# Kernel tuning notes

Measured on AMD Instinct MI355X. Metric: run time of the kernel, lower is better.

The kernel has to match this reference:

```python
import jax, jax.numpy as jnp
import numpy as np

B, T_TEXT, T_MEL = 8, 256, 1024
VOCAB, MEL, H = 256, 80, 512
NH, HD = 8, 64  # MultiheadAttention: 8 heads, head_dim 64


def _linear(x, w, b):
    return x @ w.T + b


def _lstm(x, w_ih, w_hh, b_ih, b_hh, reverse=False):
    # torch LSTM, gate order i,f,g,o; x: [B,T,Din] -> [B,T,H]
    xg = jnp.einsum('bti,gi->btg', x, w_ih) + b_ih  # precompute input contributions
    h0 = jnp.zeros((x.shape[0], w_hh.shape[1]), x.dtype)

    def step(carry, xt):
        h, c = carry
        g = xt + h @ w_hh.T + b_hh
        i, f, gg, o = jnp.split(g, 4, axis=-1)
        c = jax.nn.sigmoid(f) * c + jax.nn.sigmoid(i) * jnp.tanh(gg)
        h = jax.nn.sigmoid(o) * jnp.tanh(c)
        return (h, c), h

    _, hs = jax.lax.scan(step, (h0, h0), jnp.swapaxes(xg, 0, 1), reverse=reverse)
    return jnp.swapaxes(hs, 0, 1)


def _length_regulate(enc, durations, max_len):
    # Vectorized equivalent of the nested python loop: token j owns output
    # positions [cum[j-1], cum[j]); padded positions are zero, mask True=pad.
    dur = jnp.round(durations).astype(jnp.int32)
    cum = jnp.cumsum(dur, axis=1)                              # [B,T_text]
    pos = jnp.arange(max_len)                                  # [max_len]
    idx = jax.vmap(lambda c: jnp.searchsorted(c, pos, side='right'))(cum)
    pad_mask = pos[None, :] >= cum[:, -1:]                     # True = padded
    idx = jnp.minimum(idx, enc.shape[1] - 1)
    exp = jnp.take_along_axis(enc, idx[..., None], axis=1)     # [B,max_len,H]
    exp = exp * (~pad_mask)[..., None].astype(enc.dtype)
    return exp, pad_mask


def setup_inputs() -> dict:
    key = jax.random.key(0)
    ks = jax.random.split(key, 40)

    def rn(k, shape, scale=0.02):
        return jax.random.normal(k, shape, jnp.float32) * scale

    inp = {}
    inp['phoneme_indices'] = jax.random.randint(ks[0], (B, T_TEXT), 0, VOCAB)
    inp['mel_specs'] = jax.random.normal(ks[1], (B, T_MEL, MEL), jnp.float32)
    inp['phoneme_durations'] = jax.random.randint(ks[2], (B, T_TEXT), 0, 8).astype(jnp.float32)
    # parameters
    inp['emb'] = rn(ks[3], (VOCAB, H), 1.0)
    inp['enc_w_ih_f'] = rn(ks[4], (4 * H, H))
    inp['enc_w_hh_f'] = rn(ks[5], (4 * H, H))
    inp['enc_b_ih_f'] = rn(ks[6], (4 * H,))
    inp['enc_b_hh_f'] = rn(ks[7], (4 * H,))
    inp['enc_w_ih_b'] = rn(ks[8], (4 * H, H))
    inp['enc_w_hh_b'] = rn(ks[9], (4 * H, H))
    inp['enc_b_ih_b'] = rn(ks[10], (4 * H,))
    inp['enc_b_hh_b'] = rn(ks[11], (4 * H,))
    inp['proj_w'] = rn(ks[12], (H, 2 * H))
    inp['proj_b'] = rn(ks[13], (H,))
    inp['dur_w1'] = rn(ks[14], (H, H))
    inp['dur_b1'] = rn(ks[15], (H,))
    inp['dur_w2'] = rn(ks[16], (H // 2, H))
    inp['dur_b2'] = rn(ks[17], (H // 2,))
    inp['dur_w3'] = rn(ks[18], (1, H // 2))
    inp['dur_b3'] = rn(ks[19], (1,))
    inp['mel_in_w'] = rn(ks[20], (H, MEL))
    inp['mel_in_b'] = rn(ks[21], (H,))
    inp['attn_in_w'] = rn(ks[22], (3 * H, H))
    inp['attn_in_b'] = rn(ks[23], (3 * H,))
    inp['attn_out_w'] = rn(ks[24], (H, H))
    inp['attn_out_b'] = rn(ks[25], (H,))
    inp['dec_w_ih'] = rn(ks[26], (4 * H, 2 * H))
    inp['dec_w_hh'] = rn(ks[27], (4 * H, H))
    inp['dec_b_ih'] = rn(ks[28], (4 * H,))
    inp['dec_b_hh'] = rn(ks[29], (4 * H,))
    inp['mel_out_w'] = rn(ks[30], (MEL, H))
    inp['mel_out_b'] = rn(ks[31], (MEL,))
    return inp


def reference(phoneme_indices, mel_specs, phoneme_durations, emb,
              enc_w_ih_f, enc_w_hh_f, enc_b_ih_f, enc_b_hh_f,
              enc_w_ih_b, enc_w_hh_b, enc_b_ih_b, enc_b_hh_b,
              proj_w, proj_b, dur_w1, dur_b1, dur_w2, dur_b2, dur_w3, dur_b3,
              mel_in_w, mel_in_b, attn_in_w, attn_in_b, attn_out_w, attn_out_b,
              dec_w_ih, dec_w_hh, dec_b_ih, dec_b_hh, mel_out_w, mel_out_b):
    b = phoneme_indices.shape[0]
    # encode_text (dropout = identity in eval)
    x = emb[phoneme_indices]                                   # [B,T_text,H]
    hf = _lstm(x, enc_w_ih_f, enc_w_hh_f, enc_b_ih_f, enc_b_hh_f)
    hb = _lstm(x, enc_w_ih_b, enc_w_hh_b, enc_b_ih_b, enc_b_hh_b, reverse=True)
    enc = _linear(jnp.concatenate([hf, hb], axis=-1), proj_w, proj_b)
    # duration predictor
    h1 = jax.nn.relu(_linear(enc, dur_w1, dur_b1))
    h2 = jax.nn.relu(_linear(h1, dur_w2, dur_b2))
    log_dur = _linear(h2, dur_w3, dur_b3)[..., 0]              # [B,T_text]
    # length regulation to mel length
    exp, pad_mask = _length_regulate(enc, phoneme_durations, mel_specs.shape[1])
    # teacher-forced decoder: queries depend only on shifted mel targets,
    # so the per-timestep attention loop == one batched MHA over all steps.
    mel_in = jnp.concatenate([jnp.zeros_like(mel_specs[:, :1]), mel_specs[:, :-1]], axis=1)
    q_in = _linear(mel_in, mel_in_w, mel_in_b)                 # [B,T_mel,H]
    wq, wk, wv = jnp.split(attn_in_w, 3, axis=0)
    bq, bk, bv = jnp.split(attn_in_b, 3, axis=0)
    q = _linear(q_in, wq, bq).reshape(b, -1, NH, HD)
    k = _linear(exp, wk, bk).reshape(b, -1, NH, HD)
    v = _linear(exp, wv, bv).reshape(b, -1, NH, HD)
    scores = jnp.einsum('bqhd,bkhd->bhqk', q, k) / np.sqrt(HD).astype(np.float32)
    scores = jnp.where(pad_mask[:, None, None, :], jnp.asarray(-1e9, scores.dtype), scores)
    attn = jax.nn.softmax(scores, axis=-1)
    ctx = jnp.einsum('bhqk,bkhd->bqhd', attn, v).reshape(b, -1, H)
    attended = _linear(ctx, attn_out_w, attn_out_b)
    # decoder LSTM over full sequence (the only true recurrence)
    dec_in = jnp.concatenate([q_in, attended], axis=-1)        # [B,T_mel,2H]
    dec_out = _lstm(dec_in, dec_w_ih, dec_w_hh, dec_b_ih, dec_b_hh)
    mel_pred = _linear(dec_out, mel_out_w, mel_out_b)          # [B,T_mel,MEL]
    return mel_pred, log_dur
```

## Files before the change

### kernel.cpp

```cpp
#include <hip/hip_runtime.h>
#include <hip/hip_bf16.h>


typedef unsigned short u16;
typedef unsigned int u32;
typedef unsigned long long u64;
typedef short short8 __attribute__((ext_vector_type(8)));
typedef float float4_ __attribute__((ext_vector_type(4)));

__device__ __forceinline__ u16 f2b16(float f) {
  u32 u = __float_as_uint(f);
  u = (u + 0x7FFF + ((u >> 16) & 1)) >> 16;
  return (u16)u;
}
__device__ __forceinline__ float b2f(u16 h) { return __uint_as_float((u32)h << 16); }
__device__ __forceinline__ float sigm(float x) { return 1.f / (1.f + __expf(-x)); }
__device__ __forceinline__ float tanh_(float x) { return 2.f / (1.f + __expf(-2.f * x)) - 1.f; }

__global__ void f2b_k(const float* __restrict__ s, u16* __restrict__ d, int n) {
  for (int i = blockIdx.x * 256 + threadIdx.x; i < n; i += gridDim.x * 256) d[i] = f2b16(s[i]);
}
__global__ void permconv_k(const float* __restrict__ s, u16* __restrict__ d, int K) {
  int row = blockIdx.x; int u = row >> 2, G = row & 3;
  const float* sr = s + (long)(G * 512 + u) * K;
  u16* dr = d + (long)row * K;
  for (int c = threadIdx.x; c < K; c += 256) dr[c] = f2b16(sr[c]);
}
__global__ void biascomb_k(const float* __restrict__ bih, const float* __restrict__ bhh,
                           float* __restrict__ out) {
  int r = blockIdx.x * 256 + threadIdx.x;
  int u = r >> 2, G = r & 3;
  out[r] = bih[G * 512 + u] + bhh[G * 512 + u];
}
__global__ void melinw_k(const float* __restrict__ s, u16* __restrict__ d) {
  int row = blockIdx.x, c = threadIdx.x;
  d[row * 128 + c] = (c < 80) ? f2b16(s[row * 80 + c]) : (u16)0;
}
__global__ void meloutw_k(const float* __restrict__ s, u16* __restrict__ d) {
  int row = blockIdx.x;
  for (int c = threadIdx.x; c < 512; c += 256)
    d[row * 512 + c] = (row < 80) ? f2b16(s[row * 512 + c]) : (u16)0;
}
__global__ void biaspad_k(const float* __restrict__ s, float* __restrict__ d) {
  int t = threadIdx.x;
  d[t] = (t < 80) ? s[t] : 0.f;
}
__global__ void embed_k(const int* __restrict__ pid, const float* __restrict__ emb,
                        u16* __restrict__ x) {
  int t = blockIdx.x, b = blockIdx.y;
  int row = pid[b * 256 + t];
  const float* e = emb + (long)row * 512;
  u16* xr = x + ((long)b * 256 + t) * 512;
  xr[threadIdx.x] = f2b16(e[threadIdx.x]);
  xr[threadIdx.x + 256] = f2b16(e[threadIdx.x + 256]);
}
__global__ void melin_k(const float* __restrict__ mel, u16* __restrict__ out) {
  int t = blockIdx.x, b = blockIdx.y, c = threadIdx.x;
  float v = (c < 80 && t > 0) ? mel[((long)b * 1024 + (t - 1)) * 80 + c] : 0.f;
  out[((long)b * 1024 + t) * 128 + c] = f2b16(v);
}
__global__ void cumsum_k(const float* __restrict__ dur, int* __restrict__ cum,
                         int* __restrict__ Lb) {
  int b = blockIdx.x, t = threadIdx.x;
  __shared__ int sd[256];
  sd[t] = __float2int_rn(dur[b * 256 + t]);
  __syncthreads();
  for (int o = 1; o < 256; o <<= 1) {
    int v = (t >= o) ? sd[t - o] : 0;
    __syncthreads();
    sd[t] += v;
    __syncthreads();
  }
  cum[b * 256 + t] = sd[t];
  if (t == 255) Lb[b] = min(sd[255], 1024);
}
__global__ void gather_k(const int* __restrict__ cum, const u16* __restrict__ enc,
                         u16* __restrict__ exp_) {
  int pos = blockIdx.x, b = blockIdx.y;
  const int* cb = cum + b * 256;
  int last = cb[255];
  u32 val = 0;
  if (pos < last) {
    int lo = 0, hi = 255;
    while (lo < hi) { int mid = (lo + hi) >> 1; if (cb[mid] > pos) hi = mid; else lo = mid + 1; }
    val = ((const u32*)(enc + ((long)b * 256 + lo) * 512))[threadIdx.x];
  }
  ((u32*)(exp_ + ((long)b * 1024 + pos) * 512))[threadIdx.x] = val;
}
__global__ void softmax_k(const float* __restrict__ sbuf, u16* __restrict__ P,
                          const int* __restrict__ Lb) {
  int qp = blockIdx.x, b = blockIdx.y;
  const float* s = sbuf + ((long)b * 1024 + qp) * 1024;
  u16* p = P + ((long)b * 1024 + qp) * 1024;
  int L = Lb[b];
  __shared__ float red[256];
  int tid = threadIdx.x;
  float m = -1e30f;
  for (int i = tid; i < L; i += 256) m = fmaxf(m, s[i]);
  red[tid] = m; __syncthreads();
  for (int o = 128; o > 0; o >>= 1) { if (tid < o) red[tid] = fmaxf(red[tid], red[tid + o]); __syncthreads(); }
  float mx = red[0];
  __syncthreads();
  float sm = 0.f;
  for (int i = tid; i < L; i += 256) sm += __expf(s[i] - mx);
  red[tid] = sm; __syncthreads();
  for (int o = 128; o > 0; o >>= 1) { if (tid < o) red[tid] += red[tid + o]; __syncthreads(); }
  float inv = 1.f / red[0];
  for (int i = tid; i < 1024; i += 256) {
    float v = (i < L) ? __expf(s[i] - mx) * inv : 0.f;
    p[i] = f2b16(v);
  }
}
__global__ void dur3_k(const u16* __restrict__ h2, const float* __restrict__ w3,
                       const float* __restrict__ b3, float* __restrict__ out) {
  int row = blockIdx.x * 4 + (threadIdx.x >> 6);
  int l = threadIdx.x & 63;
  const u16* hr = h2 + (long)row * 256;
  float s = 0.f;
  for (int i = 0; i < 4; i++) { int c = l * 4 + i; s += b2f(hr[c]) * w3[c]; }
  for (int o = 32; o > 0; o >>= 1) s += __shfl_down(s, o);
  if (l == 0) out[row] = s + b3[0];
}

__global__ __launch_bounds__(256) void gemm_bt(
    const u16* __restrict__ A, const u16* __restrict__ A2, int ksplit, int lda, int lda2, long sA,
    const u16* __restrict__ B, int ldb, long sB, void* __restrict__ Cv, int ldc, long sC,
    const float* __restrict__ bias, float alpha, int N, int K, int flags) {
  __shared__ u16 As[128 * 72];
  __shared__ u16 Bs[128 * 72];
  int z = blockIdx.z;
  const u16* Ab = A + (long)z * sA;
  const u16* A2b = A2 ? (A2 + (long)z * sA) : (const u16*)0;
  const u16* Bb = B + (long)z * sB;
  int m0 = blockIdx.x * 128, n0 = blockIdx.y * 128;
  int tid = threadIdx.x, wave = tid >> 6, lane = tid & 63;
  int wm = wave & 1, wn = wave >> 1;
  int nl = lane & 15, kb = (lane >> 4) * 8, ml = (lane >> 4) * 4;
  float4_ acc[4][4];
  for (int i = 0; i < 4; i++)
    for (int j = 0; j < 4; j++) { acc[i][j][0] = 0; acc[i][j][1] = 0; acc[i][j][2] = 0; acc[i][j][3] = 0; }
  int rr = tid >> 3, cc = (tid & 7) * 8;
  for (int k0 = 0; k0 < K; k0 += 64) {
    int gk = k0 + cc;
#pragma unroll
    for (int i = 0; i < 4; i++) {
      int row = rr + i * 32;
      const u16* sa = (gk < ksplit) ? (Ab + (long)(m0 + row) * lda + gk)
                                    : (A2b + (long)(m0 + row) * lda2 + (gk - ksplit));
      *(short8*)&As[row * 72 + cc] = *(const short8*)sa;
      *(short8*)&Bs[row * 72 + cc] = *(const short8*)(Bb + (long)(n0 + row) * ldb + gk);
    }
    __syncthreads();
#pragma unroll
    for (int kk = 0; kk < 64; kk += 32) {
      short8 af[4], bfr[4];
#pragma unroll
      for (int i = 0; i < 4; i++) af[i] = *(const short8*)&As[(wm * 64 + i * 16 + nl) * 72 + kk + kb];
#pragma unroll
      for (int i = 0; i < 4; i++) bfr[i] = *(const short8*)&Bs[(wn * 64 + i * 16 + nl) * 72 + kk + kb];
#pragma unroll
      for (int mi = 0; mi < 4; mi++)
#pragma unroll
        for (int ni = 0; ni < 4; ni++)
          acc[mi][ni] = __builtin_amdgcn_mfma_f32_16x16x32_bf16(af[mi], bfr[ni], acc[mi][ni], 0, 0, 0);
    }
    __syncthreads();
  }
  for (int ni = 0; ni < 4; ni++) {
    int n = n0 + wn * 64 + ni * 16 + nl;
    if (n >= N) continue;
    float bv = bias ? bias[n] : 0.f;
    for (int mi = 0; mi < 4; mi++) {
#pragma unroll
      for (int r = 0; r < 4; r++) {
        int m = m0 + wm * 64 + mi * 16 + ml + r;
        float v = acc[mi][ni][r] * alpha + bv;
        if (flags & 2) v = fmaxf(v, 0.f);
        long idx = (flags & 4) ? ((long)n * ldc + m) : ((long)m * ldc + n);
        if (flags & 1) ((u16*)Cv)[z * sC + idx] = f2b16(v);
        else ((float*)Cv)[z * sC + idx] = v;
      }
    }
  }
}


__global__ __launch_bounds__(256) void enc_rec_k(
    const float* __restrict__ xg_f, const float* __restrict__ xg_b,
    const u16* __restrict__ whh_f, const u16* __restrict__ whh_b,
    u16* __restrict__ hcat, u64* __restrict__ hglob) {
  int dir = blockIdx.x >> 5, wg = blockIdx.x & 31;
  int tid = threadIdx.x, wave = tid >> 6, lane = tid & 63;
  int nl = lane & 15, kb = (lane >> 4) * 8, ml = (lane >> 4) * 4;
  int nt = wg * 4 + wave;
  const float* xg = dir ? xg_b : xg_f;
  const u16* whh = dir ? whh_b : whh_f;
  u64* hg = hglob + dir * 4096;
  __shared__ u16 w_s[64 * 520];
  __shared__ u16 h_s[2][16 * 520];
  __shared__ float gbuf[4][16][17];
  __shared__ float c_s[4][4][8];
  for (int i = tid; i < 64 * 64; i += 256) {
    int g = i >> 6, col = (i & 63) * 8;
    *(short8*)&w_s[g * 520 + col] = *(const short8*)(whh + (long)(wg * 64 + g) * 512 + col);
  }
  if (lane < 32) c_s[wave][lane & 3][lane >> 2] = 0.f;
  __syncthreads();
  float nxt[4];
  {
    int t0 = dir ? 255 : 0;
#pragma unroll
    for (int r = 0; r < 4; r++) {
      int m = ml + r;
      nxt[r] = (m < 8) ? xg[((long)m * 256 + t0) * 2048 + nt * 16 + nl] : 0.f;
    }
  }
  const u16* wrow = w_s + (wave * 16 + nl) * 520 + kb;
  int prow = tid >> 5, c32 = tid & 31;
  for (int s = 0; s < 256; ++s) {
    int t = dir ? 255 - s : s;
    int pb = s & 1;
    float4_ acc, acc2;
    acc[0] = nxt[0]; acc[1] = nxt[1]; acc[2] = nxt[2]; acc[3] = nxt[3];
    acc2[0] = 0; acc2[1] = 0; acc2[2] = 0; acc2[3] = 0;
    if (s > 0) {
      const u64* hp = hg + (long)pb * 2048 + prow * 256 + c32 * 8;
      u64 a[8];
      u32 tg = (u32)s;
      for (;;) {
#pragma unroll
        for (int i = 0; i < 8; i++)
          a[i] = __hip_atomic_load(hp + i, __ATOMIC_RELAXED, __HIP_MEMORY_SCOPE_AGENT);
        u32 bad = 0;
#pragma unroll
        for (int i = 0; i < 8; i++) bad |= ((u32)(a[i] >> 32) ^ tg);
        if (!bad) break;
      }
      u64* dp = (u64*)(h_s[pb] + prow * 520 + c32 * 16);
      dp[0] = (a[0] & 0xffffffffull) | (a[1] << 32);
      dp[1] = (a[2] & 0xffffffffull) | (a[3] << 32);
      dp[2] = (a[4] & 0xffffffffull) | (a[5] << 32);
      dp[3] = (a[6] & 0xffffffffull) | (a[7] << 32);
    }
    __builtin_amdgcn_sched_barrier(0);
    if (s + 1 < 256) {
      int tn = dir ? 255 - (s + 1) : (s + 1);
#pragma unroll
      for (int r = 0; r < 4; r++) {
        int m = ml + r;
        nxt[r] = (m < 8) ? xg[((long)m * 256 + tn) * 2048 + nt * 16 + nl] : 0.f;
      }
    }
    __syncthreads();
    if (s > 0) {
      const u16* hrow = h_s[pb] + nl * 520 + kb;
#pragma unroll
      for (int kc = 0; kc < 16; kc += 2) {
        short8 a0 = *(const short8*)(hrow + kc * 32);
        short8 b0 = *(const short8*)(wrow + kc * 32);
        acc = __builtin_amdgcn_mfma_f32_16x16x32_bf16(a0, b0, acc, 0, 0, 0);
        short8 a1 = *(const short8*)(hrow + (kc + 1) * 32);
        short8 b1 = *(const short8*)(wrow + (kc + 1) * 32);
        acc2 = __builtin_amdgcn_mfma_f32_16x16x32_bf16(a1, b1, acc2, 0, 0, 0);
      }
      acc += acc2;
    }
    gbuf[wave][nl][ml + 0] = acc[0];
    gbuf[wave][nl][ml + 1] = acc[1];
    gbuf[wave][nl][ml + 2] = acc[2];
    gbuf[wave][nl][ml + 3] = acc[3];
    if (lane < 32) {
      int ul = lane & 3, b = lane >> 2;
      float gi = gbuf[wave][ul * 4 + 0][b];
      float gf = gbuf[wave][ul * 4 + 1][b];
      float gg = gbuf[wave][ul * 4 + 2][b];
      float go = gbuf[wave][ul * 4 + 3][b];
      float c = c_s[wave][ul][b];
      c = sigm(gf) * c + sigm(gi) * tanh_(gg);
      float h = sigm(go) * tanh_(c);
      c_s[wave][ul][b] = c;
      int u = nt * 4 + ul;
      u16 hb2 = f2b16(h);
      u32 partner = (u32)__shfl_down((int)hb2, 1);
      if ((ul & 1) == 0) {
        u32 pair = (u32)hb2 | (partner << 16);
        *(u32*)&hcat[((long)b * 256 + t) * 1024 + dir * 512 + u] = pair;
        u64 word = (u64)pair | ((u64)(u32)(s + 1) << 32);
        __hip_atomic_store(hg + (long)((s + 1) & 1) * 2048 + b * 256 + (u >> 1), word,
                           __ATOMIC_RELAXED, __HIP_MEMORY_SCOPE_AGENT);
      }
    }
  }
}

__global__ __launch_bounds__(256) void dec_rec_k(
    const float* __restrict__ xg, const u16* __restrict__ whh,
    u16* __restrict__ dec_out, u64* __restrict__ hglob) {
  int wg = blockIdx.x;
  int tid = threadIdx.x, wave = tid >> 6, lane = tid & 63;
  int nl = lane & 15, kb = (lane >> 4) * 8, ml = (lane >> 4) * 4;
  int nt = wg * 4 + wave;
  __shared__ u16 w_s[64 * 520];
  __shared__ u16 h_s[2][16 * 520];
  __shared__ float gbuf[4][16][17];
  __shared__ float c_s[4][4][8];
  for (int i = tid; i < 64 * 64; i += 256) {
    int g = i >> 6, col = (i & 63) * 8;
    *(short8*)&w_s[g * 520 + col] = *(const short8*)(whh + (long)(wg * 64 + g) * 512 + col);
  }
  if (lane < 32) c_s[wave][lane & 3][lane >> 2] = 0.f;
  __syncthreads();
  float nxt[4];
#pragma unroll
  for (int r = 0; r < 4; r++) {
    int m = ml + r;
    nxt[r] = (m < 8) ? xg[((long)m * 1024 + 0) * 2048 + nt * 16 + nl] : 0.f;
  }
  const u16* wrow = w_s + (wave * 16 + nl) * 520 + kb;
  int prow = tid >> 5, c32 = tid & 31;
  for (int s = 0; s < 1024; ++s) {
    int pb = s & 1;
    float4_ acc, acc2;
    acc[0] = nxt[0]; acc[1] = nxt[1]; acc[2] = nxt[2]; acc[3] = nxt[3];
    acc2[0] = 0; acc2[1] = 0; acc2[2] = 0; acc2[3] = 0;
    if (s > 0) {
      const u64* hp = hglob + (long)pb * 2048 + prow * 256 + c32 * 8;
      u64 a[8];
      u32 tg = (u32)s;
      for (;;) {
#pragma unroll
        for (int i = 0; i < 8; i++)
          a[i] = __hip_atomic_load(hp + i, __ATOMIC_RELAXED, __HIP_MEMORY_SCOPE_AGENT);
        u32 bad = 0;
#pragma unroll
        for (int i = 0; i < 8; i++) bad |= ((u32)(a[i] >> 32) ^ tg);
        if (!bad) break;
      }
      u64* dp = (u64*)(h_s[pb] + prow * 520 + c32 * 16);
      dp[0] = (a[0] & 0xffffffffull) | (a[1] << 32);
      dp[1] = (a[2] & 0xffffffffull) | (a[3] << 32);
      dp[2] = (a[4] & 0xffffffffull) | (a[5] << 32);
      dp[3] = (a[6] & 0xffffffffull) | (a[7] << 32);
    }
    __builtin_amdgcn_sched_barrier(0);
    if (s + 1 < 1024) {
#pragma unroll
      for (int r = 0; r < 4; r++) {
        int m = ml + r;
        nxt[r] = (m < 8) ? xg[((long)m * 1024 + (s + 1)) * 2048 + nt * 16 + nl] : 0.f;
      }
    }
    __syncthreads();
    if (s > 0) {
      const u16* hrow = h_s[pb] + nl * 520 + kb;
#pragma unroll
      for (int kc = 0; kc < 16; kc += 2) {
        short8 a0 = *(const short8*)(hrow + kc * 32);
        short8 b0 = *(const short8*)(wrow + kc * 32);
        acc = __builtin_amdgcn_mfma_f32_16x16x32_bf16(a0, b0, acc, 0, 0, 0);
        short8 a1 = *(const short8*)(hrow + (kc + 1) * 32);
        short8 b1 = *(const short8*)(wrow + (kc + 1) * 32);
        acc2 = __builtin_amdgcn_mfma_f32_16x16x32_bf16(a1, b1, acc2, 0, 0, 0);
      }
      acc += acc2;
    }
    gbuf[wave][nl][ml + 0] = acc[0];
    gbuf[wave][nl][ml + 1] = acc[1];
    gbuf[wave][nl][ml + 2] = acc[2];
    gbuf[wave][nl][ml + 3] = acc[3];
    if (lane < 32) {
      int ul = lane & 3, b = lane >> 2;
      float gi = gbuf[wave][ul * 4 + 0][b];
      float gf = gbuf[wave][ul * 4 + 1][b];
      float gg = gbuf[wave][ul * 4 + 2][b];
      float go = gbuf[wave][ul * 4 + 3][b];
      float c = c_s[wave][ul][b];
      c = sigm(gf) * c + sigm(gi) * tanh_(gg);
      float h = sigm(go) * tanh_(c);
      c_s[wave][ul][b] = c;
      int u = nt * 4 + ul;
      u16 hb2 = f2b16(h);
      u32 partner = (u32)__shfl_down((int)hb2, 1);
      if ((ul & 1) == 0) {
        u32 pair = (u32)hb2 | (partner << 16);
        *(u32*)&dec_out[((long)b * 1024 + s) * 512 + u] = pair;
        u64 word = (u64)pair | ((u64)(u32)(s + 1) << 32);
        __hip_atomic_store(hglob + (long)((s + 1) & 1) * 2048 + b * 256 + (u >> 1), word,
                           __ATOMIC_RELAXED, __HIP_MEMORY_SCOPE_AGENT);
      }
    }
  }
}

extern "C" void kernel_launch(void* const* d_in, const int* in_sizes, int n_in,
                              void* d_out, int out_size, void* d_ws, size_t ws_size,
                              hipStream_t stream) {
  (void)in_sizes; (void)n_in; (void)out_size; (void)ws_size;
  const int* pid = (const int*)d_in[0];
  const float* mel = (const float*)d_in[1];
  const float* dur = (const float*)d_in[2];
  const float* emb = (const float*)d_in[3];
  const float* e_ihf = (const float*)d_in[4];
  const float* e_hhf = (const float*)d_in[5];
  const float* e_bihf = (const float*)d_in[6];
  const float* e_bhhf = (const float*)d_in[7];
  const float* e_ihb = (const float*)d_in[8];
  const float* e_hhb = (const float*)d_in[9];
  const float* e_bihb = (const float*)d_in[10];
  const float* e_bhhb = (const float*)d_in[11];
  const float* proj_w = (const float*)d_in[12];
  const float* proj_b = (const float*)d_in[13];
  const float* dw1 = (const float*)d_in[14];
  const float* db1 = (const float*)d_in[15];
  const float* dw2 = (const float*)d_in[16];
  const float* db2 = (const float*)d_in[17];
  const float* dw3 = (const float*)d_in[18];
  const float* db3 = (const float*)d_in[19];
  const float* miw = (const float*)d_in[20];
  const float* mib = (const float*)d_in[21];
  const float* aiw = (const float*)d_in[22];
  const float* aib = (const float*)d_in[23];
  const float* aow = (const float*)d_in[24];
  const float* aob = (const float*)d_in[25];
  const float* d_ih = (const float*)d_in[26];
  const float* d_hh = (const float*)d_in[27];
  const float* d_bih = (const float*)d_in[28];
  const float* d_bhh = (const float*)d_in[29];
  const float* mow = (const float*)d_in[30];
  const float* mob = (const float*)d_in[31];
  float* out = (float*)d_out;

  char* W = (char*)d_ws;
  constexpr size_t o_xgf = 0;
  constexpr size_t o_xgb = o_xgf + 16777216;
  constexpr size_t o_sbuf = o_xgb + 16777216;
  constexpr size_t o_decxg = o_xgf;
  constexpr size_t o_pool = o_sbuf + 33554432;
  constexpr size_t o_x = o_pool;
  constexpr size_t o_hcat = o_x + 2097152;
  constexpr size_t o_dh1 = o_hcat + 4194304;
  constexpr size_t o_dh2 = o_dh1 + 2097152;
  constexpr size_t o_melin = o_dh2 + 1048576;
  constexpr size_t o_att = o_pool;
  constexpr size_t o_enc = o_melin + 2097152;
  constexpr size_t o_exp = o_enc + 2097152;
  constexpr size_t o_ctx = o_exp;
  constexpr size_t o_qin = o_exp + 8388608;
  constexpr size_t o_q = o_qin + 8388608;
  constexpr size_t o_decout = o_q;
  constexpr size_t o_k = o_q + 8388608;
  constexpr size_t o_vt = o_k + 8388608;
  constexpr size_t o_p = o_vt + 8519680;
  constexpr size_t o_w0 = o_p + 16777216;
  constexpr size_t o_w_eihf = o_w0;
  constexpr size_t o_w_eihb = o_w_eihf + 2097152;
  constexpr size_t o_w_ehhf = o_w_eihb + 2097152;
  constexpr size_t o_w_ehhb = o_w_ehhf + 2097152;
  constexpr size_t o_w_dih = o_w_ehhb + 2097152;
  constexpr size_t o_w_dhh = o_w_dih + 4194304;
  constexpr size_t o_w_proj = o_w_dhh + 2097152;
  constexpr size_t o_w_d1 = o_w_proj + 1048576;
  constexpr size_t o_w_d2 = o_w_d1 + 524288;
  constexpr size_t o_w_ai = o_w_d2 + 262144;
  constexpr size_t o_w_ao = o_w_ai + 1572864;
  constexpr size_t o_w_mi = o_w_ao + 524288;
  constexpr size_t o_w_mo = o_w_mi + 131072;
  constexpr size_t o_bc_ef = o_w_mo + 131072;
  constexpr size_t o_bc_eb = o_bc_ef + 8192;
  constexpr size_t o_bc_d = o_bc_eb + 8192;
  constexpr size_t o_b_mo = o_bc_d + 8192;
  constexpr size_t o_cum = o_b_mo + 512;
  constexpr size_t o_lb = o_cum + 8192;
  constexpr size_t o_hge = o_lb + 256;
  constexpr size_t o_hgd = o_hge + 65536;

  hipMemsetAsync(W + o_hge, 0, 98304, stream);

  f2b_k<<<512, 256, 0, stream>>>(proj_w, (u16*)(W + o_w_proj), 512 * 1024);
  f2b_k<<<512, 256, 0, stream>>>(dw1, (u16*)(W + o_w_d1), 512 * 512);
  f2b_k<<<256, 256, 0, stream>>>(dw2, (u16*)(W + o_w_d2), 256 * 512);
  f2b_k<<<512, 256, 0, stream>>>(aiw, (u16*)(W + o_w_ai), 1536 * 512);
  f2b_k<<<512, 256, 0, stream>>>(aow, (u16*)(W + o_w_ao), 512 * 512);
  permconv_k<<<2048, 256, 0, stream>>>(e_ihf, (u16*)(W + o_w_eihf), 512);
  permconv_k<<<2048, 256, 0, stream>>>(e_ihb, (u16*)(W + o_w_eihb), 512);
  permconv_k<<<2048, 256, 0, stream>>>(e_hhf, (u16*)(W + o_w_ehhf), 512);
  permconv_k<<<2048, 256, 0, stream>>>(e_hhb, (u16*)(W + o_w_ehhb), 512);
  permconv_k<<<2048, 256, 0, stream>>>(d_ih, (u16*)(W + o_w_dih), 1024);
  permconv_k<<<2048, 256, 0, stream>>>(d_hh, (u16*)(W + o_w_dhh), 512);
  biascomb_k<<<8, 256, 0, stream>>>(e_bihf, e_bhhf, (float*)(W + o_bc_ef));
  biascomb_k<<<8, 256, 0, stream>>>(e_bihb, e_bhhb, (float*)(W + o_bc_eb));
  biascomb_k<<<8, 256, 0, stream>>>(d_bih, d_bhh, (float*)(W + o_bc_d));
  melinw_k<<<512, 128, 0, stream>>>(miw, (u16*)(W + o_w_mi));
  meloutw_k<<<128, 256, 0, stream>>>(mow, (u16*)(W + o_w_mo));
  biaspad_k<<<1, 128, 0, stream>>>(mob, (float*)(W + o_b_mo));

  auto gemm = [&](size_t oA, size_t oA2, int ksplit, int lda, int lda2, long sA, size_t oB,
                  int ldb, long sB, void* C, int ldc, long sC, const float* bias, float alpha,
                  int M, int N, int K, int flags, int batch) {
    dim3 g(M / 128, (N + 127) / 128, batch);
    gemm_bt<<<g, 256, 0, stream>>>((const u16*)(W + oA),
                                   oA2 ? (const u16*)(W + oA2) : (const u16*)0, ksplit, lda, lda2,
                                   sA, (const u16*)(W + oB), ldb, sB, C, ldc, sC, bias, alpha, N,
                                   K, flags);
  };

  embed_k<<<dim3(256, 8), 256, 0, stream>>>(pid, emb, (u16*)(W + o_x));
  gemm(o_x, 0, 512, 512, 0, 0, o_w_eihf, 512, 0, W + o_xgf, 2048, 0,
       (const float*)(W + o_bc_ef), 1.f, 2048, 2048, 512, 0, 1);
  gemm(o_x, 0, 512, 512, 0, 0, o_w_eihb, 512, 0, W + o_xgb, 2048, 0,
       (const float*)(W + o_bc_eb), 1.f, 2048, 2048, 512, 0, 1);
  enc_rec_k<<<64, 256, 0, stream>>>((const float*)(W + o_xgf), (const float*)(W + o_xgb),
                                    (const u16*)(W + o_w_ehhf), (const u16*)(W + o_w_ehhb),
                                    (u16*)(W + o_hcat), (u64*)(W + o_hge));
  gemm(o_hcat, 0, 1024, 1024, 0, 0, o_w_proj, 1024, 0, W + o_enc, 512, 0, proj_b, 1.f, 2048, 512,
       1024, 1, 1);
  gemm(o_enc, 0, 512, 512, 0, 0, o_w_d1, 512, 0, W + o_dh1, 512, 0, db1, 1.f, 2048, 512, 512, 3, 1);
  gemm(o_dh1, 0, 512, 512, 0, 0, o_w_d2, 512, 0, W + o_dh2, 256, 0, db2, 1.f, 2048, 256, 512, 3, 1);
  dur3_k<<<512, 256, 0, stream>>>((const u16*)(W + o_dh2), dw3, db3, out + 655360);
  cumsum_k<<<8, 256, 0, stream>>>(dur, (int*)(W + o_cum), (int*)(W + o_lb));
  gather_k<<<dim3(1024, 8), 256, 0, stream>>>((const int*)(W + o_cum), (const u16*)(W + o_enc),
                                              (u16*)(W + o_exp));
  melin_k<<<dim3(1024, 8), 128, 0, stream>>>(mel, (u16*)(W + o_melin));
  gemm(o_melin, 0, 128, 128, 0, 0, o_w_mi, 128, 0, W + o_qin, 512, 0, mib, 1.f, 8192, 512, 128, 1, 1);
  gemm(o_qin, 0, 512, 512, 0, 0, o_w_ai, 512, 0, W + o_q, 512, 0, aib, 1.f, 8192, 512, 512, 1, 1);
  gemm(o_exp, 0, 512, 512, 0, 0, o_w_ai + (size_t)512 * 512 * 2, 512, 0, W + o_k, 512, 0,
       aib + 512, 1.f, 8192, 512, 512, 1, 1);
  gemm(o_exp, 0, 512, 512, 0, 524288, o_w_ai + (size_t)1024 * 512 * 2, 512, 0, W + o_vt, 1024,
       524288, aib + 1024, 1.f, 1024, 512, 512, 5, 8);
  for (int h = 0; h < 8; h++) {
    gemm(o_q + (size_t)h * 128, 0, 64, 512, 0, 524288, o_k + (size_t)h * 128, 512, 524288,
         W + o_sbuf, 1024, 1048576, (const float*)0, 0.125f, 1024, 1024, 64, 0, 8);
    softmax_k<<<dim3(1024, 8), 256, 0, stream>>>((const float*)(W + o_sbuf), (u16*)(W + o_p),
                                                 (const int*)(W + o_lb));
    gemm(o_p, 0, 1024, 1024, 0, 1048576, o_vt + (size_t)h * 64 * 1024 * 2, 1024, 524288,
         (u16*)(W + o_ctx) + h * 64, 512, 524288, (const float*)0, 1.f, 1024, 64, 1024, 1, 8);
  }
  gemm(o_ctx, 0, 512, 512, 0, 0, o_w_ao, 512, 0, W + o_att, 512, 0, aob, 1.f, 8192, 512, 512, 1, 1);
  gemm(o_qin, o_att, 512, 512, 512, 0, o_w_dih, 1024, 0, W + o_decxg, 2048, 0,
       (const float*)(W + o_bc_d), 1.f, 8192, 2048, 1024, 0, 1);
  dec_rec_k<<<32, 256, 0, stream>>>((const float*)(W + o_decxg), (const u16*)(W + o_w_dhh),
                                    (u16*)(W + o_decout), (u64*)(W + o_hgd));
  gemm(o_decout, 0, 512, 512, 0, 0, o_w_mo, 512, 0, d_out, 80, 0, (const float*)(W + o_b_mo), 1.f,
       8192, 80, 512, 0, 1);
}
```

Measured before the change: 3.721 ms.

## Add dedicated loader wave to poll global hidden state in LSTM recurrences

Both recurrent kernels (encoder and decoder) now launch a fifth wavefront. It alone spin-polls the tagged global hidden-state buffer and writes the previous step's h into the double-buffered shared memory. The four compute waves no longer do the atomic polling; they only wait at the per-step barrier and then run the MFMA and gate math. The aim is to separate inter-block synchronisation from compute. The cost is that a single wave must pull all 2048 tagged words per step, which lengthens the load on the critical path. Correctness also depends on barrier counts matching between the loader wave and the compute waves.

```diff
diff --git a/kernel.cpp b/kernel.cpp
--- a/kernel.cpp
+++ b/kernel.cpp
@@ -185,14 +185,12 @@
 }
 
 
-__global__ __launch_bounds__(256) void enc_rec_k(
+__global__ __launch_bounds__(320) void enc_rec_k(
     const float* __restrict__ xg_f, const float* __restrict__ xg_b,
     const u16* __restrict__ whh_f, const u16* __restrict__ whh_b,
     u16* __restrict__ hcat, u64* __restrict__ hglob) {
   int dir = blockIdx.x >> 5, wg = blockIdx.x & 31;
   int tid = threadIdx.x, wave = tid >> 6, lane = tid & 63;
-  int nl = lane & 15, kb = (lane >> 4) * 8, ml = (lane >> 4) * 4;
-  int nt = wg * 4 + wave;
   const float* xg = dir ? xg_b : xg_f;
   const u16* whh = dir ? whh_b : whh_f;
   u64* hg = hglob + dir * 4096;
@@ -200,12 +198,41 @@
   __shared__ u16 h_s[2][16 * 520];
   __shared__ float gbuf[4][16][17];
   __shared__ float c_s[4][4][8];
-  for (int i = tid; i < 64 * 64; i += 256) {
+  for (int i = tid; i < 64 * 64; i += 320) {
     int g = i >> 6, col = (i & 63) * 8;
     *(short8*)&w_s[g * 520 + col] = *(const short8*)(whh + (long)(wg * 64 + g) * 512 + col);
   }
-  if (lane < 32) c_s[wave][lane & 3][lane >> 2] = 0.f;
+  if (wave < 4 && lane < 32) c_s[wave][lane & 3][lane >> 2] = 0.f;
   __syncthreads();
+  if (wave == 4) {
+    for (int s = 0; s < 256; ++s) {
+      int pb = s & 1;
+      if (s > 0) {
+        const u64* hp = hg + (long)pb * 2048 + lane;
+        u32 tg = (u32)s;
+        u64 a[32];
+        for (;;) {
+#pragma unroll
+          for (int i = 0; i < 32; i++)
+            a[i] = __hip_atomic_load(hp + i * 64, __ATOMIC_RELAXED, __HIP_MEMORY_SCOPE_AGENT);
+          u32 bad = 0;
+#pragma unroll
+          for (int i = 0; i < 32; i++) bad |= ((u32)(a[i] >> 32) ^ tg);
+          if (!bad) break;
+        }
+        u32* hs32 = (u32*)&h_s[pb][0];
+#pragma unroll
+        for (int i = 0; i < 32; i++) {
+          int w = i * 64 + lane;
+          hs32[(w >> 8) * 260 + (w & 255)] = (u32)a[i];
+        }
+      }
+      __syncthreads();
+    }
+    return;
+  }
+  int nl = lane & 15, kb = (lane >> 4) * 8, ml = (lane >> 4) * 4;
+  int nt = wg * 4 + wave;
   float nxt[4];
   {
     int t0 = dir ? 255 : 0;
@@ -216,33 +243,12 @@
     }
   }
   const u16* wrow = w_s + (wave * 16 + nl) * 520 + kb;
-  int prow = tid >> 5, c32 = tid & 31;
   for (int s = 0; s < 256; ++s) {
     int t = dir ? 255 - s : s;
     int pb = s & 1;
     float4_ acc, acc2;
     acc[0] = nxt[0]; acc[1] = nxt[1]; acc[2] = nxt[2]; acc[3] = nxt[3];
     acc2[0] = 0; acc2[1] = 0; acc2[2] = 0; acc2[3] = 0;
-    if (s > 0) {
-      const u64* hp = hg + (long)pb * 2048 + prow * 256 + c32 * 8;
-      u64 a[8];
-      u32 tg = (u32)s;
-      for (;;) {
-#pragma unroll
-        for (int i = 0; i < 8; i++)
-          a[i] = __hip_atomic_load(hp + i, __ATOMIC_RELAXED, __HIP_MEMORY_SCOPE_AGENT);
-        u32 bad = 0;
-#pragma unroll
-        for (int i = 0; i < 8; i++) bad |= ((u32)(a[i] >> 32) ^ tg);
-        if (!bad) break;
-      }
-      u64* dp = (u64*)(h_s[pb] + prow * 520 + c32 * 16);
-      dp[0] = (a[0] & 0xffffffffull) | (a[1] << 32);
-      dp[1] = (a[2] & 0xffffffffull) | (a[3] << 32);
-      dp[2] = (a[4] & 0xffffffffull) | (a[5] << 32);
-      dp[3] = (a[6] & 0xffffffffull) | (a[7] << 32);
-    }
-    __builtin_amdgcn_sched_barrier(0);
     if (s + 1 < 256) {
       int tn = dir ? 255 - (s + 1) : (s + 1);
 #pragma unroll
@@ -293,23 +299,50 @@
   }
 }
 
-__global__ __launch_bounds__(256) void dec_rec_k(
+__global__ __launch_bounds__(320) void dec_rec_k(
     const float* __restrict__ xg, const u16* __restrict__ whh,
     u16* __restrict__ dec_out, u64* __restrict__ hglob) {
   int wg = blockIdx.x;
   int tid = threadIdx.x, wave = tid >> 6, lane = tid & 63;
-  int nl = lane & 15, kb = (lane >> 4) * 8, ml = (lane >> 4) * 4;
-  int nt = wg * 4 + wave;
   __shared__ u16 w_s[64 * 520];
   __shared__ u16 h_s[2][16 * 520];
   __shared__ float gbuf[4][16][17];
   __shared__ float c_s[4][4][8];
-  for (int i = tid; i < 64 * 64; i += 256) {
+  for (int i = tid; i < 64 * 64; i += 320) {
     int g = i >> 6, col = (i & 63) * 8;
     *(short8*)&w_s[g * 520 + col] = *(const short8*)(whh + (long)(wg * 64 + g) * 512 + col);
   }
-  if (lane < 32) c_s[wave][lane & 3][lane >> 2] = 0.f;
+  if (wave < 4 && lane < 32) c_s[wave][lane & 3][lane >> 2] = 0.f;
   __syncthreads();
+  if (wave == 4) {
+    for (int s = 0; s < 1024; ++s) {
+      int pb = s & 1;
+      if (s > 0) {
+        const u64* hp = hglob + (long)pb * 2048 + lane;
+        u32 tg = (u32)s;
+        u64 a[32];
+        for (;;) {
+#pragma unroll
+          for (int i = 0; i < 32; i++)
+            a[i] = __hip_atomic_load(hp + i * 64, __ATOMIC_RELAXED, __HIP_MEMORY_SCOPE_AGENT);
+          u32 bad = 0;
+#pragma unroll
+          for (int i = 0; i < 32; i++) bad |= ((u32)(a[i] >> 32) ^ tg);
+          if (!bad) break;
+        }
+        u32* hs32 = (u32*)&h_s[pb][0];
+#pragma unroll
+        for (int i = 0; i < 32; i++) {
+          int w = i * 64 + lane;
+          hs32[(w >> 8) * 260 + (w & 255)] = (u32)a[i];
+        }
+      }
+      __syncthreads();
+    }
+    return;
+  }
+  int nl = lane & 15, kb = (lane >> 4) * 8, ml = (lane >> 4) * 4;
+  int nt = wg * 4 + wave;
   float nxt[4];
 #pragma unroll
   for (int r = 0; r < 4; r++) {
@@ -317,32 +350,11 @@
     nxt[r] = (m < 8) ? xg[((long)m * 1024 + 0) * 2048 + nt * 16 + nl] : 0.f;
   }
   const u16* wrow = w_s + (wave * 16 + nl) * 520 + kb;
-  int prow = tid >> 5, c32 = tid & 31;
   for (int s = 0; s < 1024; ++s) {
     int pb = s & 1;
     float4_ acc, acc2;
     acc[0] = nxt[0]; acc[1] = nxt[1]; acc[2] = nxt[2]; acc[3] = nxt[3];
     acc2[0] = 0; acc2[1] = 0; acc2[2] = 0; acc2[3] = 0;
-    if (s > 0) {
-      const u64* hp = hglob + (long)pb * 2048 + prow * 256 + c32 * 8;
-      u64 a[8];
-      u32 tg = (u32)s;
-      for (;;) {
-#pragma unroll
-        for (int i = 0; i < 8; i++)
-          a[i] = __hip_atomic_load(hp + i, __ATOMIC_RELAXED, __HIP_MEMORY_SCOPE_AGENT);
-        u32 bad = 0;
-#pragma unroll
-        for (int i = 0; i < 8; i++) bad |= ((u32)(a[i] >> 32) ^ tg);
-        if (!bad) break;
-      }
-      u64* dp = (u64*)(h_s[pb] + prow * 520 + c32 * 16);
-      dp[0] = (a[0] & 0xffffffffull) | (a[1] << 32);
-      dp[1] = (a[2] & 0xffffffffull) | (a[3] << 32);
-      dp[2] = (a[4] & 0xffffffffull) | (a[5] << 32);
-      dp[3] = (a[6] & 0xffffffffull) | (a[7] << 32);
-    }
-    __builtin_amdgcn_sched_barrier(0);
     if (s + 1 < 1024) {
 #pragma unroll
       for (int r = 0; r < 4; r++) {
@@ -509,7 +521,7 @@
        (const float*)(W + o_bc_ef), 1.f, 2048, 2048, 512, 0, 1);
   gemm(o_x, 0, 512, 512, 0, 0, o_w_eihb, 512, 0, W + o_xgb, 2048, 0,
        (const float*)(W + o_bc_eb), 1.f, 2048, 2048, 512, 0, 1);
-  enc_rec_k<<<64, 256, 0, stream>>>((const float*)(W + o_xgf), (const float*)(W + o_xgb),
+  enc_rec_k<<<64, 320, 0, stream>>>((const float*)(W + o_xgf), (const float*)(W + o_xgb),
                                     (const u16*)(W + o_w_ehhf), (const u16*)(W + o_w_ehhb),
                                     (u16*)(W + o_hcat), (u64*)(W + o_hge));
   gemm(o_hcat, 0, 1024, 1024, 0, 0, o_w_proj, 1024, 0, W + o_enc, 512, 0, proj_b, 1.f, 2048, 512,
@@ -538,7 +550,7 @@
   gemm(o_ctx, 0, 512, 512, 0, 0, o_w_ao, 512, 0, W + o_att, 512, 0, aob, 1.f, 8192, 512, 512, 1, 1);
   gemm(o_qin, o_att, 512, 512, 512, 0, o_w_dih, 1024, 0, W + o_decxg, 2048, 0,
        (const float*)(W + o_bc_d), 1.f, 8192, 2048, 1024, 0, 1);
-  dec_rec_k<<<32, 256, 0, stream>>>((const float*)(W + o_decxg), (const u16*)(W + o_w_dhh),
+  dec_rec_k<<<32, 320, 0, stream>>>((const float*)(W + o_decxg), (const u16*)(W + o_w_dhh),
                                     (u16*)(W + o_decout), (u64*)(W + o_hgd));
   gemm(o_decout, 0, 512, 512, 0, 0, o_w_mo, 512, 0, d_out, 80, 0, (const float*)(W + o_b_mo), 1.f,
        8192, 80, 512, 0, 1);
```

Result: slower. 4.834 ms (+29.9%).
